# Kernel optimization log

Measured on AMD Instinct MI355X. Metric: run time of the kernel, lower is better.

The kernel has to match this reference:

```python
import math
import jax, jax.numpy as jnp
import numpy as np

HIDDEN = 1024
NUM_HEADS = 16
HEAD_DIM = HIDDEN // NUM_HEADS
B, S = 4, 2048


def setup_inputs() -> dict:
    key = jax.random.key(0)
    ks = jax.random.split(key, 10)
    sc_in = 1.0 / math.sqrt(HIDDEN)
    inp = {
        "query": jax.random.normal(ks[0], (B, S, HIDDEN), jnp.float32),
        "key": jax.random.normal(ks[1], (B, S, HIDDEN), jnp.float32),
        "value": jax.random.normal(ks[2], (B, S, HIDDEN), jnp.float32),
        "mask": jax.random.randint(ks[3], (B, S), 0, 2).astype(bool),
        # NOTE: ModuleList([Linear]*num_heads) shares ONE Linear across all heads.
        "Wq": jax.random.normal(ks[4], (HIDDEN, HEAD_DIM), jnp.float32) * sc_in,
        "bq": jnp.zeros((HEAD_DIM,), jnp.float32),
        "Wk": jax.random.normal(ks[5], (HIDDEN, HEAD_DIM), jnp.float32) * sc_in,
        "bk": jnp.zeros((HEAD_DIM,), jnp.float32),
        "Wv": jax.random.normal(ks[6], (HIDDEN, HEAD_DIM), jnp.float32) * sc_in,
        "bv": jnp.zeros((HEAD_DIM,), jnp.float32),
        "Wout": jax.random.normal(ks[7], (HIDDEN, HIDDEN), jnp.float32) * sc_in,
        "bout": jnp.zeros((HIDDEN,), jnp.float32),
        "seq_mask": 0,
    }
    return inp


def _layer_norm_scores(x, eps=1e-8):
    # torch.std is unbiased (ddof=1); is_train=False => no affine
    mean = jnp.mean(x, axis=-1, keepdims=True)
    sigma = jnp.std(x, axis=-1, keepdims=True, ddof=1)
    return (x - mean) / (sigma + eps)


def reference(query, key, value, mask, Wq, bq, Wk, bk, Wv, bv, Wout, bout, seq_mask):
    # All heads share identical weights -> compute one head, tile the concat.
    q = query @ Wq + bq          # [B,S,hd]
    k = key @ Wk + bk            # [B,S,hd]
    v = value @ Wv + bv          # [B,S,hd]
    scores = jnp.einsum("bqd,bkd->bqk", q, k) / math.sqrt(HIDDEN)  # [B,S,S]
    scores = _layer_norm_scores(scores)
    m = jnp.broadcast_to(mask[:, None, :], scores.shape)  # [B,S,S]
    if seq_mask:
        tri = jnp.triu(jnp.ones(scores.shape[-2:], bool), k=1)
        m = m | tri[None]
    # original fills with -1e-32 (effectively a no-op bug) -- reproduce exactly
    scores = scores + jnp.where(m, jnp.float32(-1e-32), jnp.float32(0.0))
    attn = jax.nn.softmax(scores, axis=-1)
    head = jnp.einsum("bqk,bkd->bqd", attn, v)   # [B,S,hd]
    attention = jnp.tile(head, (1, 1, NUM_HEADS))  # concat of identical heads
    return attention @ Wout + bout
```

## Files before the change

kernel.cpp:

```cpp
#include <hip/hip_runtime.h>
#include <math.h>

#define B_  4
#define S_  2048
#define H_  1024
#define D_  64
#define ROWS (B_*S_)
#define LOG2E 1.4426950408889634f

typedef __attribute__((ext_vector_type(4))) float  floatx4;
typedef __attribute__((ext_vector_type(8))) short  short8;
typedef __attribute__((ext_vector_type(8))) __bf16 bf16x8;

#define WS_KSUM 0
#define WS_M    (WS_KSUM + B_*D_)
#define WS_FEND (WS_M + B_*D_*D_)
#define WB_QB  0
#define WB_KF  (WB_QB + ROWS*D_)
#define WB_VF  (WB_KF + ROWS*D_)
#define WB_WT  (WB_VF + ROWS*D_)
#define WB_WFF (WB_WT + 3*D_*H_)
#define NZ2    (B_*D_ + B_*D_*D_)

__device__ __forceinline__ unsigned short f2bf(float f) {
    union { float f; unsigned u; } v; v.f = f;
    unsigned r = v.u + 0x7FFFu + ((v.u >> 16) & 1u);
    return (unsigned short)(r >> 16);
}
__device__ __forceinline__ short bfc(float f) {
    __bf16 h = (__bf16)f;
    short s; __builtin_memcpy(&s, &h, 2); return s;
}
__device__ __forceinline__ float bf2f(short s) {
    union { unsigned u; float f; } v;
    v.u = ((unsigned)(unsigned short)s) << 16; return v.f;
}
__device__ __forceinline__ bf16x8 ldb(const short* p) {
    union { short8 s; bf16x8 b; } u; u.s = *(const short8*)p; return u.b;
}
__device__ __forceinline__ bf16x8 s2b(short8 s) {
    union { short8 s; bf16x8 b; } u; u.s = s; return u.b;
}
#define MFMA(a,b,c) __builtin_amdgcn_mfma_f32_16x16x32_bf16(a, b, c, 0, 0, 0)
__device__ __forceinline__ void lds_fence() {
    __builtin_amdgcn_wave_barrier();
    __builtin_amdgcn_s_waitcnt(0xc07f);
    __builtin_amdgcn_wave_barrier();
}

__global__ __launch_bounds__(256) void prep(
    const float* __restrict__ Wq, const float* __restrict__ Wk,
    const float* __restrict__ Wv, const float* __restrict__ Wout,
    float* __restrict__ wsf)
{
    __shared__ float tile[64][65];
    short* wsb = (short*)(wsf + WS_FEND);
    const int bx = blockIdx.x, t = threadIdx.x;
    if (bx < 96) {
        int idx = bx * 256 + t;
        int mat = idx >> 13, rem = idx & 8191;
        int kc = rem >> 8, nt = (rem >> 6) & 3, lane = rem & 63;
        int g = lane >> 4, l15 = lane & 15;
        const float* W = (mat == 0) ? Wq : (mat == 1) ? Wk : Wv;
        short8 fr;
        #pragma unroll
        for (int j = 0; j < 8; ++j)
            fr[j] = (short)f2bf(W[(size_t)(kc*32 + g*8 + j) * D_ + nt*16 + l15]);
        *(short8*)&wsb[WB_WT + (size_t)idx * 8] = fr;
    } else if (bx < 112) {
        int n0 = (bx - 96) * 64;
        int nn = t & 63, dg = t >> 6;
        for (int dd = 0; dd < 16; ++dd) {
            int d = dg * 16 + dd;
            float s = 0.0f;
            #pragma unroll
            for (int h = 0; h < 16; ++h)
                s += Wout[(size_t)(h * 64 + d) * H_ + n0 + nn];
            tile[d][nn] = s;
        }
        __syncthreads();
        #pragma unroll
        for (int u = 0; u < 2; ++u) {
            int s = 2*t + u;
            int ctl = s >> 7, h = (s >> 6) & 1, lane = s & 63;
            int g = lane >> 4, l2 = lane & 15;
            short8 fr;
            #pragma unroll
            for (int j = 0; j < 8; ++j)
                fr[j] = (short)f2bf(tile[h*32 + g*8 + j][ctl*16 + l2]);
            *(short8*)&wsb[WB_WFF + (size_t)((((n0 >> 4) + ctl)*2 + h)*64 + lane) * 8] = fr;
        }
    } else {
        int i = (bx - 112) * 256 + t;
        if (i < NZ2) wsf[WS_KSUM + i] = 0.0f;
    }
}

__global__ __launch_bounds__(256) void qkv_mfma(
    const float* __restrict__ query, const float* __restrict__ key,
    const float* __restrict__ value,
    const float* __restrict__ bq, const float* __restrict__ bk,
    const float* __restrict__ bvp, float* __restrict__ wsf)
{
    short* wsb = (short*)(wsf + WS_FEND);
    const int mat = blockIdx.y;
    const float* X    = (mat == 0) ? query : (mat == 1) ? key : value;
    const float* bias = (mat == 0) ? bq    : (mat == 1) ? bk  : bvp;
    const short* WT3 = wsb + WB_WT + (size_t)mat * (D_ * H_);

    const int t = threadIdx.x, w = t >> 6, lane = t & 63;
    const int l15 = lane & 15, g = lane >> 4;
    const int r0 = blockIdx.x * 32;
    const int mrow0 = (w >> 1) * 16;
    const int nt0 = (w & 1) * 2;

    __shared__ short xs[2][32][136];
    __shared__ float kf[32][65];
    floatx4 acc[2] = {};

    const int lrow = t >> 5;
    const int lcol = (t & 31) * 4;
    float4 rr[4];
    #pragma unroll
    for (int u = 0; u < 4; ++u)
        rr[u] = *(const float4*)&X[(size_t)(r0 + u*8 + lrow) * H_ + lcol];

    for (int step = 0; step < 8; ++step) {
        const int p = step & 1;
        __syncthreads();
        #pragma unroll
        for (int u = 0; u < 4; ++u) {
            short4 pk;
            pk.x = bfc(rr[u].x); pk.y = bfc(rr[u].y);
            pk.z = bfc(rr[u].z); pk.w = bfc(rr[u].w);
            *(short4*)&xs[p][u*8 + lrow][lcol] = pk;
        }
        if (step < 7) {
            #pragma unroll
            for (int u = 0; u < 4; ++u)
                rr[u] = *(const float4*)&X[(size_t)(r0 + u*8 + lrow) * H_ + (step+1) * 128 + lcol];
        }
        __syncthreads();
        #pragma unroll
        for (int kk = 0; kk < 4; ++kk) {
            bf16x8 a = ldb(&xs[p][mrow0 + l15][kk * 32 + g * 8]);
            int kc = step * 4 + kk;
            #pragma unroll
            for (int n = 0; n < 2; ++n) {
                bf16x8 bf = ldb(&WT3[(size_t)((kc * 4) + nt0 + n) * 512 + lane * 8]);
                acc[n] = MFMA(a, bf, acc[n]);
            }
        }
    }

    if (mat == 0) {
        short* QB = wsb + WB_QB;
        #pragma unroll
        for (int n = 0; n < 2; ++n) {
            int col = (nt0 + n) * 16 + l15;
            float bb = bias[col];
            #pragma unroll
            for (int r = 0; r < 4; ++r)
                QB[(size_t)(r0 + mrow0 + 4*g + r) * D_ + col] = (short)f2bf(acc[n][r] + bb);
        }
    } else if (mat == 1) {
        short* KFp = wsb + WB_KF;
        #pragma unroll
        for (int n = 0; n < 2; ++n) {
            int d = (nt0 + n) * 16 + l15;
            int kh = d >> 5, gk = (d >> 3) & 3, j = d & 7;
            float bb = bias[d];
            #pragma unroll
            for (int r = 0; r < 4; ++r) {
                int R = r0 + mrow0 + 4*g + r;
                unsigned short hv = f2bf(acc[n][r] + bb);
                KFp[(size_t)(((R >> 4) * 2 + kh) * 64 + gk * 16 + (R & 15)) * 8 + j] =
                    (short)hv;
                kf[mrow0 + 4*g + r][d] = bf2f((short)hv);
            }
        }
        __syncthreads();
        const int b = r0 >> 11;
        const int gj = g * 8;
        short8 ts;
        bf16x8 fb[4];
        #pragma unroll
        for (int i = 0; i < 4; ++i) {
            #pragma unroll
            for (int j = 0; j < 8; ++j)
                ts[j] = bfc(kf[gj + j][i*16 + l15]);
            fb[i] = s2b(ts);
        }
        #pragma unroll
        for (int j = 0; j < 8; ++j)
            ts[j] = bfc(kf[gj + j][w*16 + l15]);
        bf16x8 fa = s2b(ts);
        float* M = wsf + WS_M + (size_t)b * D_ * D_;
        #pragma unroll
        for (int i2 = 0; i2 < 4; ++i2) {
            floatx4 z = {};
            floatx4 mt = MFMA(fa, fb[i2], z);
            #pragma unroll
            for (int r = 0; r < 4; ++r)
                atomicAdd(&M[(size_t)(w*16 + 4*g + r) * D_ + i2*16 + l15], mt[r]);
        }
        if (t < 64) {
            float s = 0.0f;
            #pragma unroll
            for (int jj = 0; jj < 32; ++jj) s += kf[jj][t];
            atomicAdd(&wsf[WS_KSUM + b * D_ + t], s);
        }
    } else {
        short* VF = wsb + WB_VF;
        int R0 = r0 + mrow0 + 4*g;
        int kh = (R0 >> 5) & 1, gv = (R0 >> 3) & 3, j0 = R0 & 7, blk = R0 >> 6;
        #pragma unroll
        for (int n = 0; n < 2; ++n) {
            int d = (nt0 + n) * 16 + l15;
            int ntv = d >> 4;
            float bb = bias[d];
            short4 pk;
            pk.x = (short)f2bf(acc[n][0] + bb); pk.y = (short)f2bf(acc[n][1] + bb);
            pk.z = (short)f2bf(acc[n][2] + bb); pk.w = (short)f2bf(acc[n][3] + bb);
            *(short4*)&VF[(size_t)(((blk * 4 + ntv) * 2 + kh) * 64 + gv * 16 + (d & 15)) * 8 + j0] = pk;
        }
    }
}

__global__ __launch_bounds__(512, 4) void attn_fused(
    const float* __restrict__ bout, float* __restrict__ wsf,
    float* __restrict__ out)
{
    short* wsb = (short*)(wsf + WS_FEND);
    const short* Qb  = wsb + WB_QB;
    const short* KF  = wsb + WB_KF;
    const short* VF  = wsb + WB_VF;
    const short* WFF = wsb + WB_WFF;

    __shared__ short P[8][16][72];
    __shared__ short OL[8][16][64];
    __shared__ float sumwL[8][16];
    __shared__ short hnF[2 * 64 * 8];
    __shared__ float smA[16], smC[16];

    const int t = threadIdx.x, w = t >> 6, lane = t & 63;
    const int l15 = lane & 15, g = lane >> 4;
    const int q0 = blockIdx.x * 16;
    const int b  = blockIdx.x >> 7;

    if (w < 4) {
        const int rw = q0 + w * 4;
        const float* M = wsf + WS_M + (size_t)b * D_ * D_;
        float qv[4], y[4] = {};
        #pragma unroll
        for (int r = 0; r < 4; ++r) qv[r] = bf2f(Qb[(size_t)(rw + r) * D_ + lane]);
        for (int d2 = 0; d2 < 64; ++d2) {
            float m = M[d2 * D_ + lane];
            #pragma unroll
            for (int r = 0; r < 4; ++r) y[r] += __shfl(qv[r], d2, 64) * m;
        }
        float kl = wsf[WS_KSUM + b * D_ + lane];
        float z[4], sv[4];
        #pragma unroll
        for (int r = 0; r < 4; ++r) { z[r] = y[r] * qv[r]; sv[r] = qv[r] * kl; }
        #pragma unroll
        for (int m = 1; m < 64; m <<= 1) {
            #pragma unroll
            for (int r = 0; r < 4; ++r) {
                z[r]  += __shfl_xor(z[r],  m, 64);
                sv[r] += __shfl_xor(sv[r], m, 64);
            }
        }
        #pragma unroll
        for (int r = 0; r < 4; ++r) {
            if (lane == r) {
                float sum   = sv[r] * (1.0f / 32.0f);
                float sumsq = z[r]  * (1.0f / 1024.0f);
                float mu  = sum * (1.0f / 2048.0f);
                float var = (sumsq - sum * sum * (1.0f / 2048.0f)) * (1.0f / 2047.0f);
                var = fmaxf(var, 0.0f);
                float inv = 1.0f / (sqrtf(var) + 1e-8f);
                smA[w*4 + r] = inv * (LOG2E / 32.0f);
                smC[w*4 + r] = -mu * inv * LOG2E;
            }
        }
    }

    bf16x8 bqf0 = ldb(&Qb[(size_t)(q0 + l15) * D_ + 0*32 + g*8]);
    bf16x8 bqf1 = ldb(&Qb[(size_t)(q0 + l15) * D_ + 1*32 + g*8]);
    __syncthreads();
    const float a2v = smA[l15];
    const float c2v = smC[l15];

    floatx4 O[4] = {};
    float sacc = 0.0f;
    short* Pw = &P[w][0][0];

    for (int kc = 0; kc < 256; kc += 64) {
        const int key0 = w * 256 + kc;
        const int kblk16 = (b * S_ + key0) >> 4;
        const int kblk64 = (b * S_ + key0) >> 6;
        floatx4 Sc[4] = {};
        __builtin_amdgcn_s_setprio(1);
        #pragma unroll
        for (int kt = 0; kt < 4; ++kt) {
            bf16x8 ak0 = ldb(&KF[(size_t)(((kblk16 + kt) * 2 + 0) * 64 + lane) * 8]);
            bf16x8 ak1 = ldb(&KF[(size_t)(((kblk16 + kt) * 2 + 1) * 64 + lane) * 8]);
            Sc[kt] = MFMA(ak0, bqf0, Sc[kt]);
            Sc[kt] = MFMA(ak1, bqf1, Sc[kt]);
        }
        __builtin_amdgcn_s_setprio(0);
        lds_fence();
        #pragma unroll
        for (int kt = 0; kt < 4; ++kt) {
            float w0 = __builtin_amdgcn_exp2f(fmaf(Sc[kt][0], a2v, c2v));
            float w1 = __builtin_amdgcn_exp2f(fmaf(Sc[kt][1], a2v, c2v));
            float w2 = __builtin_amdgcn_exp2f(fmaf(Sc[kt][2], a2v, c2v));
            float w3 = __builtin_amdgcn_exp2f(fmaf(Sc[kt][3], a2v, c2v));
            sacc += (w0 + w1) + (w2 + w3);
            short4 pk;
            pk.x = bfc(w0); pk.y = bfc(w1); pk.z = bfc(w2); pk.w = bfc(w3);
            *(short4*)&Pw[l15 * 72 + kt*16 + 4*g] = pk;
        }
        lds_fence();
        bf16x8 ap0 = ldb(&Pw[l15 * 72 + 0*32 + g*8]);
        bf16x8 ap1 = ldb(&Pw[l15 * 72 + 1*32 + g*8]);
        __builtin_amdgcn_s_setprio(1);
        #pragma unroll
        for (int nt = 0; nt < 4; ++nt) {
            bf16x8 bv0 = ldb(&VF[(size_t)(((kblk64 * 4 + nt) * 2 + 0) * 64 + lane) * 8]);
            bf16x8 bv1 = ldb(&VF[(size_t)(((kblk64 * 4 + nt) * 2 + 1) * 64 + lane) * 8]);
            O[nt] = MFMA(ap0, bv0, O[nt]);
            O[nt] = MFMA(ap1, bv1, O[nt]);
        }
        __builtin_amdgcn_s_setprio(0);
    }

    sacc += __shfl_xor(sacc, 16, 64);
    sacc += __shfl_xor(sacc, 32, 64);
    if (lane < 16) sumwL[w][lane] = sacc;
    #pragma unroll
    for (int nt = 0; nt < 4; ++nt)
        #pragma unroll
        for (int r = 0; r < 4; ++r)
            OL[w][4*g + r][nt*16 + l15] = (short)f2bf(O[nt][r]);
    __syncthreads();

    {
        const int row = t >> 5;
        const int c = (t & 31) * 2;
        float s0 = 0.f, s1 = 0.f, sw = 0.f;
        #pragma unroll
        for (int p = 0; p < 8; ++p) {
            s0 += bf2f(OL[p][row][c]);
            s1 += bf2f(OL[p][row][c + 1]);
            sw += sumwL[p][row];
        }
        float inv = 1.0f / sw;
        short2 hn;
        hn.x = (short)f2bf(s0 * inv);
        hn.y = (short)f2bf(s1 * inv);
        int kh = c >> 5, g2 = (c >> 3) & 3, j = c & 7;
        *(short2*)&hnF[(kh * 64 + g2 * 16 + row) * 8 + j] = hn;
    }
    __syncthreads();

    bf16x8 ah0 = ldb(&hnF[(0 * 64 + lane) * 8]);
    bf16x8 ah1 = ldb(&hnF[(1 * 64 + lane) * 8]);
    #pragma unroll
    for (int i = 0; i < 8; ++i) {
        int n16 = w * 8 + i;
        floatx4 acc = {};
        acc = MFMA(ah0, ldb(&WFF[(size_t)(n16 * 2 + 0) * 512 + lane * 8]), acc);
        acc = MFMA(ah1, ldb(&WFF[(size_t)(n16 * 2 + 1) * 512 + lane * 8]), acc);
        int col = n16 * 16 + l15;
        float bb = bout[col];
        #pragma unroll
        for (int r = 0; r < 4; ++r)
            out[(size_t)(q0 + 4*g + r) * H_ + col] = acc[r] + bb;
    }
}

extern "C" void kernel_launch(void* const* d_in, const int* in_sizes, int n_in,
                              void* d_out, int out_size, void* d_ws, size_t ws_size,
                              hipStream_t stream) {
    const float* query = (const float*)d_in[0];
    const float* key   = (const float*)d_in[1];
    const float* value = (const float*)d_in[2];
    const float* Wq   = (const float*)d_in[4];
    const float* bq   = (const float*)d_in[5];
    const float* Wk   = (const float*)d_in[6];
    const float* bk   = (const float*)d_in[7];
    const float* Wv   = (const float*)d_in[8];
    const float* bv   = (const float*)d_in[9];
    const float* Wout = (const float*)d_in[10];
    const float* bout = (const float*)d_in[11];

    float* ws  = (float*)d_ws;
    float* out = (float*)d_out;

    prep<<<177, 256, 0, stream>>>(Wq, Wk, Wv, Wout, ws);
    qkv_mfma<<<dim3(ROWS/32, 3), 256, 0, stream>>>(query, key, value, bq, bk, bv, ws);
    attn_fused<<<ROWS/16, 512, 0, stream>>>(bout, ws, out);
}
```

Measured before the change: 189.0 us.

## Process 32 queries per attention block and deepen QKV input prefetch

Each attention block now handles 32 query rows instead of 16, so every K and V fragment loaded from global memory feeds two MFMA tiles and every Wout fragment is reused across two row tiles. This halves the grid and the redundant K/V/Wout traffic per query, at the cost of more registers and LDS per block (launch bounds lowered to 2 blocks per SM). The QKV projection kernel also switches to double register buffers so loads run two steps ahead of the bf16 store and MFMA phases, at the cost of extra barriers.

```diff
diff --git a/kernel.cpp b/kernel.cpp
--- a/kernel.cpp
+++ b/kernel.cpp
@@ -120,27 +120,23 @@
 
     const int lrow = t >> 5;
     const int lcol = (t & 31) * 4;
-    float4 rr[4];
-    #pragma unroll
-    for (int u = 0; u < 4; ++u)
-        rr[u] = *(const float4*)&X[(size_t)(r0 + u*8 + lrow) * H_ + lcol];
-
-    for (int step = 0; step < 8; ++step) {
-        const int p = step & 1;
-        __syncthreads();
+    const float* Xb = &X[(size_t)r0 * H_];
+
+    auto LD = [&](float4* r, int step) {
+        #pragma unroll
+        for (int u = 0; u < 4; ++u)
+            r[u] = *(const float4*)&Xb[(size_t)(u*8 + lrow) * H_ + step * 128 + lcol];
+    };
+    auto ST = [&](const float4* r, int p) {
         #pragma unroll
         for (int u = 0; u < 4; ++u) {
             short4 pk;
-            pk.x = bfc(rr[u].x); pk.y = bfc(rr[u].y);
-            pk.z = bfc(rr[u].z); pk.w = bfc(rr[u].w);
+            pk.x = bfc(r[u].x); pk.y = bfc(r[u].y);
+            pk.z = bfc(r[u].z); pk.w = bfc(r[u].w);
             *(short4*)&xs[p][u*8 + lrow][lcol] = pk;
         }
-        if (step < 7) {
-            #pragma unroll
-            for (int u = 0; u < 4; ++u)
-                rr[u] = *(const float4*)&X[(size_t)(r0 + u*8 + lrow) * H_ + (step+1) * 128 + lcol];
-        }
-        __syncthreads();
+    };
+    auto MM = [&](int p, int step) {
         #pragma unroll
         for (int kk = 0; kk < 4; ++kk) {
             bf16x8 a = ldb(&xs[p][mrow0 + l15][kk * 32 + g * 8]);
@@ -151,6 +147,22 @@
                 acc[n] = MFMA(a, bf, acc[n]);
             }
         }
+    };
+
+    float4 ra[4], rb[4];
+    LD(ra, 0); LD(rb, 1);
+    #pragma unroll
+    for (int s2 = 0; s2 < 4; ++s2) {
+        __syncthreads();
+        ST(ra, 0);
+        if (s2 < 3) LD(ra, 2*s2 + 2);
+        __syncthreads();
+        MM(0, 2*s2);
+        __syncthreads();
+        ST(rb, 1);
+        if (s2 < 3) LD(rb, 2*s2 + 3);
+        __syncthreads();
+        MM(1, 2*s2 + 1);
     }
 
     if (mat == 0) {
@@ -227,7 +239,7 @@
     }
 }
 
-__global__ __launch_bounds__(512, 4) void attn_fused(
+__global__ __launch_bounds__(512, 2) void attn_fused(
     const float* __restrict__ bout, float* __restrict__ wsf,
     float* __restrict__ out)
 {
@@ -237,18 +249,18 @@
     const short* VF  = wsb + WB_VF;
     const short* WFF = wsb + WB_WFF;
 
-    __shared__ short P[8][16][72];
-    __shared__ short OL[8][16][64];
-    __shared__ float sumwL[8][16];
-    __shared__ short hnF[2 * 64 * 8];
-    __shared__ float smA[16], smC[16];
+    __shared__ short P[8][32][72];
+    __shared__ short OL[8][32][64];
+    __shared__ float sumwL[8][32];
+    __shared__ short hnF[2*2*64*8];
+    __shared__ float smA[32], smC[32];
 
     const int t = threadIdx.x, w = t >> 6, lane = t & 63;
     const int l15 = lane & 15, g = lane >> 4;
-    const int q0 = blockIdx.x * 16;
-    const int b  = blockIdx.x >> 7;
-
-    if (w < 4) {
+    const int q0 = blockIdx.x * 32;
+    const int b  = blockIdx.x >> 6;
+
+    {
         const int rw = q0 + w * 4;
         const float* M = wsf + WS_M + (size_t)b * D_ * D_;
         float qv[4], y[4] = {};
@@ -286,98 +298,134 @@
         }
     }
 
-    bf16x8 bqf0 = ldb(&Qb[(size_t)(q0 + l15) * D_ + 0*32 + g*8]);
-    bf16x8 bqf1 = ldb(&Qb[(size_t)(q0 + l15) * D_ + 1*32 + g*8]);
+    bf16x8 bqf[2][2];
+    #pragma unroll
+    for (int nt = 0; nt < 2; ++nt)
+        #pragma unroll
+        for (int h = 0; h < 2; ++h)
+            bqf[nt][h] = ldb(&Qb[(size_t)(q0 + nt*16 + l15) * D_ + h*32 + g*8]);
     __syncthreads();
-    const float a2v = smA[l15];
-    const float c2v = smC[l15];
-
-    floatx4 O[4] = {};
-    float sacc = 0.0f;
+    const float a2v[2] = { smA[l15], smA[16 + l15] };
+    const float c2v[2] = { smC[l15], smC[16 + l15] };
+
+    floatx4 O[2][4] = {};
+    float sacc[2] = {0.0f, 0.0f};
     short* Pw = &P[w][0][0];
 
     for (int kc = 0; kc < 256; kc += 64) {
         const int key0 = w * 256 + kc;
         const int kblk16 = (b * S_ + key0) >> 4;
         const int kblk64 = (b * S_ + key0) >> 6;
-        floatx4 Sc[4] = {};
+        floatx4 Sc[4][2] = {};
         __builtin_amdgcn_s_setprio(1);
         #pragma unroll
         for (int kt = 0; kt < 4; ++kt) {
             bf16x8 ak0 = ldb(&KF[(size_t)(((kblk16 + kt) * 2 + 0) * 64 + lane) * 8]);
             bf16x8 ak1 = ldb(&KF[(size_t)(((kblk16 + kt) * 2 + 1) * 64 + lane) * 8]);
-            Sc[kt] = MFMA(ak0, bqf0, Sc[kt]);
-            Sc[kt] = MFMA(ak1, bqf1, Sc[kt]);
+            #pragma unroll
+            for (int nt = 0; nt < 2; ++nt) {
+                Sc[kt][nt] = MFMA(ak0, bqf[nt][0], Sc[kt][nt]);
+                Sc[kt][nt] = MFMA(ak1, bqf[nt][1], Sc[kt][nt]);
+            }
         }
         __builtin_amdgcn_s_setprio(0);
         lds_fence();
         #pragma unroll
-        for (int kt = 0; kt < 4; ++kt) {
-            float w0 = __builtin_amdgcn_exp2f(fmaf(Sc[kt][0], a2v, c2v));
-            float w1 = __builtin_amdgcn_exp2f(fmaf(Sc[kt][1], a2v, c2v));
-            float w2 = __builtin_amdgcn_exp2f(fmaf(Sc[kt][2], a2v, c2v));
-            float w3 = __builtin_amdgcn_exp2f(fmaf(Sc[kt][3], a2v, c2v));
-            sacc += (w0 + w1) + (w2 + w3);
-            short4 pk;
-            pk.x = bfc(w0); pk.y = bfc(w1); pk.z = bfc(w2); pk.w = bfc(w3);
-            *(short4*)&Pw[l15 * 72 + kt*16 + 4*g] = pk;
+        for (int nt = 0; nt < 2; ++nt) {
+            const float aa = a2v[nt], cc = c2v[nt];
+            #pragma unroll
+            for (int kt = 0; kt < 4; ++kt) {
+                float w0 = __builtin_amdgcn_exp2f(fmaf(Sc[kt][nt][0], aa, cc));
+                float w1 = __builtin_amdgcn_exp2f(fmaf(Sc[kt][nt][1], aa, cc));
+                float w2 = __builtin_amdgcn_exp2f(fmaf(Sc[kt][nt][2], aa, cc));
+                float w3 = __builtin_amdgcn_exp2f(fmaf(Sc[kt][nt][3], aa, cc));
+                sacc[nt] += (w0 + w1) + (w2 + w3);
+                short4 pk;
+                pk.x = bfc(w0); pk.y = bfc(w1); pk.z = bfc(w2); pk.w = bfc(w3);
+                *(short4*)&Pw[(nt*16 + l15) * 72 + kt*16 + 4*g] = pk;
+            }
         }
         lds_fence();
-        bf16x8 ap0 = ldb(&Pw[l15 * 72 + 0*32 + g*8]);
-        bf16x8 ap1 = ldb(&Pw[l15 * 72 + 1*32 + g*8]);
+        bf16x8 ap[2][2];
+        #pragma unroll
+        for (int mt = 0; mt < 2; ++mt)
+            #pragma unroll
+            for (int kh = 0; kh < 2; ++kh)
+                ap[mt][kh] = ldb(&Pw[(mt*16 + l15) * 72 + kh*32 + g*8]);
         __builtin_amdgcn_s_setprio(1);
         #pragma unroll
         for (int nt = 0; nt < 4; ++nt) {
             bf16x8 bv0 = ldb(&VF[(size_t)(((kblk64 * 4 + nt) * 2 + 0) * 64 + lane) * 8]);
             bf16x8 bv1 = ldb(&VF[(size_t)(((kblk64 * 4 + nt) * 2 + 1) * 64 + lane) * 8]);
-            O[nt] = MFMA(ap0, bv0, O[nt]);
-            O[nt] = MFMA(ap1, bv1, O[nt]);
+            #pragma unroll
+            for (int mt = 0; mt < 2; ++mt) {
+                O[mt][nt] = MFMA(ap[mt][0], bv0, O[mt][nt]);
+                O[mt][nt] = MFMA(ap[mt][1], bv1, O[mt][nt]);
+            }
         }
         __builtin_amdgcn_s_setprio(0);
     }
 
-    sacc += __shfl_xor(sacc, 16, 64);
-    sacc += __shfl_xor(sacc, 32, 64);
-    if (lane < 16) sumwL[w][lane] = sacc;
-    #pragma unroll
-    for (int nt = 0; nt < 4; ++nt)
-        #pragma unroll
-        for (int r = 0; r < 4; ++r)
-            OL[w][4*g + r][nt*16 + l15] = (short)f2bf(O[nt][r]);
+    #pragma unroll
+    for (int nt = 0; nt < 2; ++nt) {
+        sacc[nt] += __shfl_xor(sacc[nt], 16, 64);
+        sacc[nt] += __shfl_xor(sacc[nt], 32, 64);
+    }
+    if (lane < 16) {
+        sumwL[w][lane]      = sacc[0];
+        sumwL[w][16 + lane] = sacc[1];
+    }
+    #pragma unroll
+    for (int mt = 0; mt < 2; ++mt)
+        #pragma unroll
+        for (int nt = 0; nt < 4; ++nt)
+            #pragma unroll
+            for (int r = 0; r < 4; ++r)
+                OL[w][mt*16 + 4*g + r][nt*16 + l15] = (short)f2bf(O[mt][nt][r]);
     __syncthreads();
 
     {
-        const int row = t >> 5;
-        const int c = (t & 31) * 2;
-        float s0 = 0.f, s1 = 0.f, sw = 0.f;
+        const int row = t >> 4;
+        const int c = (t & 15) * 4;
+        float s0 = 0.f, s1 = 0.f, s2 = 0.f, s3 = 0.f, sw = 0.f;
         #pragma unroll
         for (int p = 0; p < 8; ++p) {
-            s0 += bf2f(OL[p][row][c]);
-            s1 += bf2f(OL[p][row][c + 1]);
+            short4 o = *(const short4*)&OL[p][row][c];
+            s0 += bf2f(o.x); s1 += bf2f(o.y); s2 += bf2f(o.z); s3 += bf2f(o.w);
             sw += sumwL[p][row];
         }
         float inv = 1.0f / sw;
-        short2 hn;
-        hn.x = (short)f2bf(s0 * inv);
-        hn.y = (short)f2bf(s1 * inv);
-        int kh = c >> 5, g2 = (c >> 3) & 3, j = c & 7;
-        *(short2*)&hnF[(kh * 64 + g2 * 16 + row) * 8 + j] = hn;
+        short4 hn;
+        hn.x = (short)f2bf(s0 * inv); hn.y = (short)f2bf(s1 * inv);
+        hn.z = (short)f2bf(s2 * inv); hn.w = (short)f2bf(s3 * inv);
+        int rb2 = row >> 4, r15 = row & 15;
+        int kh = c >> 5, g2 = (c >> 3) & 3, j0 = c & 7;
+        *(short4*)&hnF[(size_t)(((rb2*2 + kh) * 64) + g2*16 + r15) * 8 + j0] = hn;
     }
     __syncthreads();
 
-    bf16x8 ah0 = ldb(&hnF[(0 * 64 + lane) * 8]);
-    bf16x8 ah1 = ldb(&hnF[(1 * 64 + lane) * 8]);
+    bf16x8 ah[2][2];
+    #pragma unroll
+    for (int rb2 = 0; rb2 < 2; ++rb2)
+        #pragma unroll
+        for (int kh = 0; kh < 2; ++kh)
+            ah[rb2][kh] = ldb(&hnF[(size_t)((rb2*2 + kh) * 64 + lane) * 8]);
     #pragma unroll
     for (int i = 0; i < 8; ++i) {
         int n16 = w * 8 + i;
-        floatx4 acc = {};
-        acc = MFMA(ah0, ldb(&WFF[(size_t)(n16 * 2 + 0) * 512 + lane * 8]), acc);
-        acc = MFMA(ah1, ldb(&WFF[(size_t)(n16 * 2 + 1) * 512 + lane * 8]), acc);
+        bf16x8 bf0 = ldb(&WFF[(size_t)(n16 * 2 + 0) * 512 + lane * 8]);
+        bf16x8 bf1 = ldb(&WFF[(size_t)(n16 * 2 + 1) * 512 + lane * 8]);
         int col = n16 * 16 + l15;
         float bb = bout[col];
         #pragma unroll
-        for (int r = 0; r < 4; ++r)
-            out[(size_t)(q0 + 4*g + r) * H_ + col] = acc[r] + bb;
+        for (int rb2 = 0; rb2 < 2; ++rb2) {
+            floatx4 acc = {};
+            acc = MFMA(ah[rb2][0], bf0, acc);
+            acc = MFMA(ah[rb2][1], bf1, acc);
+            #pragma unroll
+            for (int r = 0; r < 4; ++r)
+                out[(size_t)(q0 + rb2*16 + 4*g + r) * H_ + col] = acc[r] + bb;
+        }
     }
 }
 
@@ -401,5 +449,5 @@
 
     prep<<<177, 256, 0, stream>>>(Wq, Wk, Wv, Wout, ws);
     qkv_mfma<<<dim3(ROWS/32, 3), 256, 0, stream>>>(query, key, value, bq, bk, bv, ws);
-    attn_fused<<<ROWS/16, 512, 0, stream>>>(bout, ws, out);
-}
+    attn_fused<<<ROWS/32, 512, 0, stream>>>(bout, ws, out);
+}
```

Measured after the change: 191.0 us. Within noise of the previous version (+1.0%).
